# Optimization experiments

Hardware: AMD Instinct MI355X
Metric: run time of the kernel (lower is better)

## Reference

```python
import jax, jax.numpy as jnp
import numpy as np

EPS = 1e-12
SLOPE = 0.2          # LeakyReLU negative slope
N_KNN = (16, 16)     # args.n_knn
TOPK = (2, 2)        # args.topk
MHC = 32             # atten_multi_head_c

def _lin(x, w):
    # VNLinear: contract channel dim (axis 1); x: [B,Cin,3,...] w: [Cout,Cin]
    return jnp.einsum('oc,bc...->bo...', w, x)

def vn_lin_lrelu(x, w, wd):
    # VNLinearAndLeakyReLU: linear + vector-neuron leaky relu with learned direction
    x = _lin(x, w)
    d = _lin(x, wd)
    dot = (x * d).sum(2, keepdims=True)
    dsq = (d * d).sum(2, keepdims=True)
    x_neg = x - (dot / (dsq + EPS)) * d
    return SLOPE * x + (1.0 - SLOPE) * jnp.where(dot >= 0, x, x_neg)

def chnorm(x):
    # channel_equi_vec_normalize: unit 3-vectors scaled by channel-normalized norms
    n = jnp.linalg.norm(x, axis=2, keepdims=True)
    x_dir = x / jnp.maximum(n, EPS)
    cn = jnp.linalg.norm(n, axis=1, keepdims=True)
    return x_dir * (n / jnp.maximum(cn, EPS))

def get_graph_feature(x, k):
    # x: [B,C,3,N] -> [B,2C,3,N,k]; knn on flattened [B,3C,N] coordinates
    B, C, _, N = x.shape
    xf = x.reshape(B, C * 3, N)
    xx = (xf * xf).sum(1)                              # [B,N]
    inner = jnp.einsum('bdn,bdm->bnm', xf, xf)
    neg_dist = 2.0 * inner - xx[:, :, None] - xx[:, None, :]
    _, idx = jax.lax.top_k(neg_dist, k)                # [B,N,k]
    xt = jnp.transpose(x, (0, 3, 1, 2))                # [B,N,C,3]
    nbr = jax.vmap(lambda t, i: t[i])(xt, idx)         # [B,N,k,C,3]
    ctr = jnp.broadcast_to(xt[:, :, None], nbr.shape)
    feat = jnp.concatenate([nbr - ctr, ctr], axis=3)   # [B,N,k,2C,3]
    return jnp.transpose(feat, (0, 3, 4, 1, 2))

def vn_dgcnn(x, w, wd, k):
    # edge conv then mean pool over neighbors
    return vn_lin_lrelu(get_graph_feature(x, k), w, wd).mean(-1)

def cross_context(x, y, qw, qd, kw, kd, vw, vd, knn_k):
    Qx = chnorm(vn_lin_lrelu(x, qw, qd))               # [B,C,3,N]
    yg = get_graph_feature(y, knn_k)                   # [B,2C,3,N,K]
    Ky = chnorm(vn_lin_lrelu(yg, kw, kd))              # [B,C,3,N,K]
    Vy = vn_lin_lrelu(yg, vw, vd)
    qk = jnp.einsum('bcdnk,bcdn->bcnk', Ky, Qx)        # [B,C,N,K]
    B, C, N, K = qk.shape
    nh = C // MHC
    logits = qk.reshape(B, nh, MHC, N, K).sum(2) / jnp.sqrt(jnp.float32(3 * MHC))
    att = jnp.repeat(jax.nn.softmax(logits, axis=-1), MHC, axis=1)  # [B,C,N,K]
    return x + jnp.einsum('bcnk,bcdnk->bcdn', att, Vy)

def _hegn(fx, fy, blocks, h_w, h_d):
    fx = fx[:, None]   # [B,1,3,N]
    fy = fy[:, None]
    fx_blocks, fy_blocks = [], []
    for i, (dg_w, dg_d, qw, qd, kw, kd, vw, vd, gw, gd) in enumerate(blocks):
        fx = vn_dgcnn(fx, dg_w, dg_d, N_KNN[i])
        fy = vn_dgcnn(fy, dg_w, dg_d, N_KNN[i])
        fx = cross_context(fx, fy, qw, qd, kw, kd, vw, vd, N_KNN[i])
        fy = cross_context(fy, fx, qw, qd, kw, kd, vw, vd, N_KNN[i])  # uses updated fx, as in torch
        Fxg = jnp.broadcast_to(fx.mean(-1, keepdims=True), fx.shape)
        Fyg = jnp.broadcast_to(fy.mean(-1, keepdims=True), fy.shape)
        fx = vn_lin_lrelu(jnp.concatenate([fx, Fxg], 1), gw, gd)
        fy = vn_lin_lrelu(jnp.concatenate([fy, Fyg], 1), gw, gd)
        fx_par = fx.mean(1, keepdims=True)             # [B,1,3,N]
        fy_par = fy.mean(1, keepdims=True)
        fx_par = fx_par / jnp.sqrt((fx_par ** 2).sum())  # torch.norm over whole tensor
        fy_par = fy_par / jnp.sqrt((fy_par ** 2).sum())
        phi_x = jnp.einsum('bcdn,bdn->bnc', fx, fx_par[:, 0])
        phi_y = jnp.einsum('bcdn,bdn->bnc', fy, fy_par[:, 0])
        Sc = jax.nn.softmax((phi_x * phi_y).sum(-1), axis=-1)   # [B,N]
        _, idx = jax.lax.top_k(Sc, Sc.shape[1] // TOPK[i])
        fx = jnp.take_along_axis(fx, idx[:, None, None, :], axis=-1)
        fy = jnp.take_along_axis(fy, idx[:, None, None, :], axis=-1)
        fx_blocks.append(fx.mean(-1))
        fy_blocks.append(fy.mean(-1))
    Fx = vn_lin_lrelu(jnp.concatenate(fx_blocks, 1), h_w, h_d)  # [B,32,3]
    Fy = vn_lin_lrelu(jnp.concatenate(fy_blocks, 1), h_w, h_d)
    H = jnp.einsum('bcd,bce->bde', Fx, Fy)                      # [B,3,3]
    u, s, vh = jnp.linalg.svd(H, full_matrices=False)
    R = u @ jnp.swapaxes(vh, -1, -2)   # torch code computes U @ V (v = vh^T)
    S = jnp.linalg.norm(Fy, axis=1) / jnp.linalg.norm(Fx, axis=1)  # [B,3]
    return R, S

def setup_inputs():
    key = jax.random.key(0)
    ks = jax.random.split(key, 26)
    def w(k, o, i):
        return jax.random.normal(k, (o, i), dtype=jnp.float32) / np.float32(np.sqrt(i))
    B, N, C = 2, 2048, 64
    return dict(
        fx=jax.random.normal(ks[0], (B, 3, N), dtype=jnp.float32),
        fy=jax.random.normal(ks[1], (B, 3, N), dtype=jnp.float32),
        dg_w0=w(ks[2], C, 2), dg_d0=w(ks[3], C, C),
        q_w0=w(ks[4], C, C), q_d0=w(ks[5], C, C),
        k_w0=w(ks[6], C, 2 * C), k_d0=w(ks[7], C, C),
        v_w0=w(ks[8], C, 2 * C), v_d0=w(ks[9], C, C),
        g_w0=w(ks[10], C, 2 * C), g_d0=w(ks[11], C, C),
        dg_w1=w(ks[12], C, 2 * C), dg_d1=w(ks[13], C, C),
        q_w1=w(ks[14], C, C), q_d1=w(ks[15], C, C),
        k_w1=w(ks[16], C, 2 * C), k_d1=w(ks[17], C, C),
        v_w1=w(ks[18], C, 2 * C), v_d1=w(ks[19], C, C),
        g_w1=w(ks[20], C, 2 * C), g_d1=w(ks[21], C, C),
        h_w=w(ks[22], 32, 2 * C), h_d=w(ks[23], 32, 32),
    )

def reference(fx, fy, dg_w0, dg_d0, q_w0, q_d0, k_w0, k_d0, v_w0, v_d0, g_w0, g_d0,
              dg_w1, dg_d1, q_w1, q_d1, k_w1, k_d1, v_w1, v_d1, g_w1, g_d1, h_w, h_d):
    blocks = [
        (dg_w0, dg_d0, q_w0, q_d0, k_w0, k_d0, v_w0, v_d0, g_w0, g_d0),
        (dg_w1, dg_d1, q_w1, q_d1, k_w1, k_d1, v_w1, v_d1, g_w1, g_d1),
    ]
    return _hegn(fx, fy, blocks, h_w, h_d)
```

## Files before the change

kernel.cpp:

```cpp
#include <hip/hip_runtime.h>
#include <math.h>

#define SLOPE 0.2f
#define EPSV 1e-12f
#define NEGINF (-3.0e38f)

static __device__ __forceinline__ float lrelu_combine(float xv, float dvv, float dot, float dsq) {
  float xneg = xv - dot / (dsq + EPSV) * dvv;
  float w = (dot >= 0.f) ? xv : xneg;
  return SLOPE * xv + (1.f - SLOPE) * w;
}

__global__ void k_xx2(const float* __restrict__ x0, const float* __restrict__ x1,
                      float* __restrict__ xxA, float* __restrict__ xxB, int D, int N) {
  int side = blockIdx.z;
  const float* x = side ? x1 : x0;
  float* xx = side ? xxB : xxA;
  int b = blockIdx.y;
  int m = blockIdx.x * 256 + threadIdx.x;
  if (m >= N) return;
  const float* xp = x + (size_t)b * D * N + m;
  float s = 0.f;
  for (int d = 0; d < D; ++d) { float v = xp[(size_t)d * N]; s = fmaf(v, v, s); }
  xx[b * N + m] = s;
}

template <int D>
__global__ void __launch_bounds__(256) k_knn2(const float* __restrict__ x0, const float* __restrict__ x1,
                                              const float* __restrict__ xxA, const float* __restrict__ xxB,
                                              int* __restrict__ idx0, int* __restrict__ idx1, int N) {
  int side = blockIdx.z;
  const float* x = side ? x1 : x0;
  const float* xx = side ? xxB : xxA;
  int* idx = side ? idx1 : idx0;
  __shared__ float qt[D * 4];
  __shared__ float dist[4][2048];
  __shared__ float xxq[4];
  int b = blockIdx.y, tid = threadIdx.x;
  int q0 = blockIdx.x * 4;
  const float* xb = x + (size_t)b * D * N;
  for (int i = tid; i < D * 4; i += 256) qt[i] = xb[(size_t)(i >> 2) * N + q0 + (i & 3)];
  if (tid < 4) xxq[tid] = xx[b * N + q0 + tid];
  __syncthreads();
  int kouter = N >> 10;
  for (int k = 0; k < kouter; ++k) {
    int m0 = tid + (k << 10);
    float4 a0 = {0, 0, 0, 0}, a1 = {0, 0, 0, 0}, a2 = {0, 0, 0, 0}, a3 = {0, 0, 0, 0};
#pragma unroll 4
    for (int d = 0; d < D; ++d) {
      const float4 q4 = *(const float4*)&qt[d * 4];
      const float* xr = xb + (size_t)d * N + m0;
      float v0 = xr[0], v1 = xr[256], v2 = xr[512], v3 = xr[768];
      a0.x = fmaf(q4.x, v0, a0.x); a0.y = fmaf(q4.y, v0, a0.y);
      a0.z = fmaf(q4.z, v0, a0.z); a0.w = fmaf(q4.w, v0, a0.w);
      a1.x = fmaf(q4.x, v1, a1.x); a1.y = fmaf(q4.y, v1, a1.y);
      a1.z = fmaf(q4.z, v1, a1.z); a1.w = fmaf(q4.w, v1, a1.w);
      a2.x = fmaf(q4.x, v2, a2.x); a2.y = fmaf(q4.y, v2, a2.y);
      a2.z = fmaf(q4.z, v2, a2.z); a2.w = fmaf(q4.w, v2, a2.w);
      a3.x = fmaf(q4.x, v3, a3.x); a3.y = fmaf(q4.y, v3, a3.y);
      a3.z = fmaf(q4.z, v3, a3.z); a3.w = fmaf(q4.w, v3, a3.w);
    }
    const float* xxb2 = xx + b * N + m0;
    float x0v = xxb2[0], x1v = xxb2[256], x2v = xxb2[512], x3v = xxb2[768];
    dist[0][m0]       = 2.f * a0.x - xxq[0] - x0v;
    dist[1][m0]       = 2.f * a0.y - xxq[1] - x0v;
    dist[2][m0]       = 2.f * a0.z - xxq[2] - x0v;
    dist[3][m0]       = 2.f * a0.w - xxq[3] - x0v;
    dist[0][m0 + 256] = 2.f * a1.x - xxq[0] - x1v;
    dist[1][m0 + 256] = 2.f * a1.y - xxq[1] - x1v;
    dist[2][m0 + 256] = 2.f * a1.z - xxq[2] - x1v;
    dist[3][m0 + 256] = 2.f * a1.w - xxq[3] - x1v;
    dist[0][m0 + 512] = 2.f * a2.x - xxq[0] - x2v;
    dist[1][m0 + 512] = 2.f * a2.y - xxq[1] - x2v;
    dist[2][m0 + 512] = 2.f * a2.z - xxq[2] - x2v;
    dist[3][m0 + 512] = 2.f * a2.w - xxq[3] - x2v;
    dist[0][m0 + 768] = 2.f * a3.x - xxq[0] - x3v;
    dist[1][m0 + 768] = 2.f * a3.y - xxq[1] - x3v;
    dist[2][m0 + 768] = 2.f * a3.z - xxq[2] - x3v;
    dist[3][m0 + 768] = 2.f * a3.w - xxq[3] - x3v;
  }
  __syncthreads();
  int g = tid >> 6, lane = tid & 63;
  float* dr = dist[g];
  int n = q0 + g;
  int imax = N >> 8;
  int* op = idx + ((size_t)b * N + n) * 16;
  for (int r = 0; r < 16; ++r) {
    float bv = NEGINF;
    int bi = N;
    for (int i = 0; i < imax; ++i) {
      int mb = i * 256 + lane * 4;
      float4 v = *(const float4*)&dr[mb];
      if (v.x > bv) { bv = v.x; bi = mb; }
      if (v.y > bv) { bv = v.y; bi = mb + 1; }
      if (v.z > bv) { bv = v.z; bi = mb + 2; }
      if (v.w > bv) { bv = v.w; bi = mb + 3; }
    }
#pragma unroll
    for (int s = 1; s < 64; s <<= 1) {
      float ov = __shfl_xor(bv, s, 64);
      int oi = __shfl_xor(bi, s, 64);
      if (ov > bv || (ov == bv && oi < bi)) { bv = ov; bi = oi; }
    }
    if (lane == 0) { op[r] = bi; dr[bi] = NEGINF; }
  }
}

struct LinSlots {
  const float* W[5]; const float* X[5]; const float* bias[5];
  float* cm[5]; float* pm[5];
  int ws[5]; int woff[5]; int sub[5];
};

template <int KT>
__global__ void __launch_bounds__(256) k_linm(LinSlots S, int N) {
  __shared__ float wl[64 * ((KT + 3) & ~3)];
  const int KP = (KT + 3) & ~3;
  int slot = blockIdx.z >> 2;
  int oc = (blockIdx.z & 3) * 16;
  const float* W = S.W[slot];
  int ws = S.ws[slot], woff = S.woff[slot], sub = S.sub[slot];
  int tid = threadIdx.x;
  for (int i = tid; i < 64 * KT; i += 256) {
    int o = i / KT, k = i - o * KT;
    float v = W[o * ws + woff + k];
    if (sub) v -= W[o * ws + k];
    wl[o * KP + k] = v;
  }
  __syncthreads();
  int b = blockIdx.y;
  int j = blockIdx.x * 256 + tid;
  int M3 = 3 * N;
  if (j >= M3) return;
  const float* Xb = S.X[slot] + (size_t)b * KT * M3;
  float xv[KT];
#pragma unroll
  for (int k = 0; k < KT; ++k) xv[k] = Xb[(size_t)k * M3 + j];
  int d = j / N;
  const float* bias = S.bias[slot];
  float acc[16];
  if (bias) {
#pragma unroll
    for (int oo = 0; oo < 16; ++oo) acc[oo] = bias[b * 192 + (oc + oo) * 3 + d];
  } else {
#pragma unroll
    for (int oo = 0; oo < 16; ++oo) acc[oo] = 0.f;
  }
#pragma unroll
  for (int oo = 0; oo < 16; ++oo) {
    const float* wr = &wl[(oc + oo) * KP];
    float s = acc[oo];
#pragma unroll
    for (int k = 0; k < KT; ++k) s = fmaf(wr[k], xv[k], s);
    acc[oo] = s;
  }
  if (S.cm[slot]) {
    float* ob = S.cm[slot] + (size_t)b * 64 * M3;
#pragma unroll
    for (int oo = 0; oo < 16; ++oo) ob[(size_t)(oc + oo) * M3 + j] = acc[oo];
  }
  if (S.pm[slot]) {
    int n = j - d * N;
    float4* pp = (float4*)(S.pm[slot] + ((size_t)((b * N + n) * 3 + d)) * 64 + oc);
    pp[0] = make_float4(acc[0], acc[1], acc[2], acc[3]);
    pp[1] = make_float4(acc[4], acc[5], acc[6], acc[7]);
    pp[2] = make_float4(acc[8], acc[9], acc[10], acc[11]);
    pp[3] = make_float4(acc[12], acc[13], acc[14], acc[15]);
  }
}

__global__ void __launch_bounds__(256) k_edge2(const float* __restrict__ P1a, const float* __restrict__ P2a,
                                               const float* __restrict__ D1a, const float* __restrict__ D2a,
                                               const float* __restrict__ P1b, const float* __restrict__ P2b,
                                               const float* __restrict__ D1b, const float* __restrict__ D2b,
                                               const int* __restrict__ idxA, const int* __restrict__ idxB,
                                               float* __restrict__ outA, float* __restrict__ outB, int N) {
  int side = blockIdx.y;
  const float* P1 = side ? P1b : P1a;
  const float* P2 = side ? P2b : P2a;
  const float* D1 = side ? D1b : D1a;
  const float* D2 = side ? D2b : D2a;
  const int* idx = side ? idxB : idxA;
  float* out = side ? outB : outA;
  int tid = threadIdx.x;
  int p = blockIdx.x * 4 + (tid >> 6);
  int c = tid & 63;
  int b = p / N, n = p - b * N;
  size_t bn = ((size_t)(b * N + n) * 3) * 64 + c;
  float p2[3], d2[3];
#pragma unroll
  for (int d = 0; d < 3; ++d) { p2[d] = P2[bn + d * 64]; d2[d] = D2[bn + d * 64]; }
  const int* ip = idx + ((size_t)b * N + n) * 16;
  float acc0 = 0.f, acc1 = 0.f, acc2 = 0.f;
  for (int j = 0; j < 16; ++j) {
    int m = ip[j];
    size_t bm = ((size_t)(b * N + m) * 3) * 64 + c;
    float xl[3], dv[3];
#pragma unroll
    for (int d = 0; d < 3; ++d) {
      xl[d] = P1[bm + d * 64] + p2[d];
      dv[d] = D1[bm + d * 64] + d2[d];
    }
    float dot = xl[0] * dv[0] + xl[1] * dv[1] + xl[2] * dv[2];
    float dsq = dv[0] * dv[0] + dv[1] * dv[1] + dv[2] * dv[2];
    acc0 += lrelu_combine(xl[0], dv[0], dot, dsq);
    acc1 += lrelu_combine(xl[1], dv[1], dot, dsq);
    acc2 += lrelu_combine(xl[2], dv[2], dot, dsq);
  }
  size_t r0 = (size_t)((b * 64 + c) * 3) * N;
  out[r0 + n] = acc0 * (1.f / 16.f);
  out[r0 + N + n] = acc1 * (1.f / 16.f);
  out[r0 + 2 * (size_t)N + n] = acc2 * (1.f / 16.f);
}

__global__ void __launch_bounds__(256) k_qfin(const float* __restrict__ XL, const float* __restrict__ DV,
                                              float* __restrict__ outpm, int N) {
  int tid = threadIdx.x;
  int p = blockIdx.x * 4 + (tid >> 6);
  int c = tid & 63;
  int b = p / N, n = p - b * N;
  size_t bn = ((size_t)(b * N + n) * 3) * 64 + c;
  float xl[3], dv[3];
#pragma unroll
  for (int d = 0; d < 3; ++d) { xl[d] = XL[bn + d * 64]; dv[d] = DV[bn + d * 64]; }
  float dot = xl[0] * dv[0] + xl[1] * dv[1] + xl[2] * dv[2];
  float dsq = dv[0] * dv[0] + dv[1] * dv[1] + dv[2] * dv[2];
  float z[3];
#pragma unroll
  for (int d = 0; d < 3; ++d) z[d] = lrelu_combine(xl[d], dv[d], dot, dsq);
  float n2 = z[0] * z[0] + z[1] * z[1] + z[2] * z[2];
  float cn2 = n2;
#pragma unroll
  for (int s = 1; s < 64; s <<= 1) cn2 += __shfl_xor(cn2, s, 64);
  float n_o = sqrtf(n2), cn = sqrtf(cn2);
  float scl = (n_o / fmaxf(cn, EPSV)) / fmaxf(n_o, EPSV);
#pragma unroll
  for (int d = 0; d < 3; ++d) outpm[bn + d * 64] = z[d] * scl;
}

__global__ void __launch_bounds__(256) k_att(const float* __restrict__ xres,
                                             const float* __restrict__ qxpm,
                                             const float* __restrict__ KP1, const float* __restrict__ KP2,
                                             const float* __restrict__ KD1, const float* __restrict__ KD2,
                                             const float* __restrict__ VP1, const float* __restrict__ VP2,
                                             const float* __restrict__ VD1, const float* __restrict__ VD2,
                                             const int* __restrict__ idx,
                                             float* __restrict__ out, int N) {
  int tid = threadIdx.x;
  int p = blockIdx.x * 4 + (tid >> 6);
  int c = tid & 63;
  int b = p / N, n = p - b * N;
  size_t bn = ((size_t)(b * N + n) * 3) * 64 + c;
  float qv[3], kp2[3], kd2[3], vp2[3], vd2[3];
#pragma unroll
  for (int d = 0; d < 3; ++d) {
    qv[d] = qxpm[bn + d * 64];
    kp2[d] = KP2[bn + d * 64];
    kd2[d] = KD2[bn + d * 64];
    vp2[d] = VP2[bn + d * 64];
    vd2[d] = VD2[bn + d * 64];
  }
  const int* ip = idx + ((size_t)b * N + n) * 16;
  float l[16];
#pragma unroll
  for (int j = 0; j < 16; ++j) {
    int m = ip[j];
    size_t bm = ((size_t)(b * N + m) * 3) * 64 + c;
    float xl[3], dv[3];
#pragma unroll
    for (int d = 0; d < 3; ++d) {
      xl[d] = KP1[bm + d * 64] + kp2[d];
      dv[d] = KD1[bm + d * 64] + kd2[d];
    }
    float dot = xl[0] * dv[0] + xl[1] * dv[1] + xl[2] * dv[2];
    float dsq = dv[0] * dv[0] + dv[1] * dv[1] + dv[2] * dv[2];
    float z[3];
#pragma unroll
    for (int d = 0; d < 3; ++d) z[d] = lrelu_combine(xl[d], dv[d], dot, dsq);
    float n2 = z[0] * z[0] + z[1] * z[1] + z[2] * z[2];
    float cn2 = n2;
#pragma unroll
    for (int s = 1; s < 64; s <<= 1) cn2 += __shfl_xor(cn2, s, 64);
    float n_o = sqrtf(n2), cn = sqrtf(cn2);
    float scl = (n_o / fmaxf(cn, EPSV)) / fmaxf(n_o, EPSV);
    float part = (z[0] * qv[0] + z[1] * qv[1] + z[2] * qv[2]) * scl;
#pragma unroll
    for (int s = 1; s < 32; s <<= 1) part += __shfl_xor(part, s, 32);
    part = __shfl(part, 0, 32);
    l[j] = part * 0.102062072615966f;
  }
  float mx = l[0];
#pragma unroll
  for (int j = 1; j < 16; ++j) mx = fmaxf(mx, l[j]);
  float sum = 0.f;
#pragma unroll
  for (int j = 0; j < 16; ++j) { l[j] = expf(l[j] - mx); sum += l[j]; }
  float inv = 1.f / sum;
#pragma unroll
  for (int j = 0; j < 16; ++j) l[j] *= inv;
  float acc0 = 0.f, acc1 = 0.f, acc2 = 0.f;
#pragma unroll
  for (int j = 0; j < 16; ++j) {
    int m = ip[j];
    float av = l[j];
    size_t bm = ((size_t)(b * N + m) * 3) * 64 + c;
    float xl[3], dv[3];
#pragma unroll
    for (int d = 0; d < 3; ++d) {
      xl[d] = VP1[bm + d * 64] + vp2[d];
      dv[d] = VD1[bm + d * 64] + vd2[d];
    }
    float dot = xl[0] * dv[0] + xl[1] * dv[1] + xl[2] * dv[2];
    float dsq = dv[0] * dv[0] + dv[1] * dv[1] + dv[2] * dv[2];
    acc0 = fmaf(av, lrelu_combine(xl[0], dv[0], dot, dsq), acc0);
    acc1 = fmaf(av, lrelu_combine(xl[1], dv[1], dot, dsq), acc1);
    acc2 = fmaf(av, lrelu_combine(xl[2], dv[2], dot, dsq), acc2);
  }
  size_t r0 = (size_t)((b * 64 + c) * 3) * N;
  out[r0 + n] = xres[r0 + n] + acc0;
  out[r0 + N + n] = xres[r0 + N + n] + acc1;
  out[r0 + 2 * (size_t)N + n] = xres[r0 + 2 * (size_t)N + n] + acc2;
}

__global__ void __launch_bounds__(256) k_gfin(const float* __restrict__ XLa, const float* __restrict__ DVa,
                                              const float* __restrict__ XLb, const float* __restrict__ DVb,
                                              float* __restrict__ outa, float* __restrict__ outpa,
                                              float* __restrict__ outb, float* __restrict__ outpb, int N) {
  int side = blockIdx.y;
  const float* XL = side ? XLb : XLa;
  const float* DV = side ? DVb : DVa;
  float* out = side ? outb : outa;
  float* outpm = side ? outpb : outpa;
  int tid = threadIdx.x;
  int p = blockIdx.x * 4 + (tid >> 6);
  int c = tid & 63;
  int b = p / N, n = p - b * N;
  size_t bn = ((size_t)(b * N + n) * 3) * 64 + c;
  float xl[3], dv[3];
#pragma unroll
  for (int d = 0; d < 3; ++d) { xl[d] = XL[bn + d * 64]; dv[d] = DV[bn + d * 64]; }
  float dot = xl[0] * dv[0] + xl[1] * dv[1] + xl[2] * dv[2];
  float dsq = dv[0] * dv[0] + dv[1] * dv[1] + dv[2] * dv[2];
  size_t r0 = (size_t)((b * 64 + c) * 3) * N;
#pragma unroll
  for (int d = 0; d < 3; ++d) {
    float z = lrelu_combine(xl[d], dv[d], dot, dsq);
    out[r0 + (size_t)d * N + n] = z;
    outpm[bn + d * 64] = z;
  }
}

__global__ void k_gbias2(const float* __restrict__ gw, const float* __restrict__ meanX,
                         const float* __restrict__ meanY,
                         float* __restrict__ cbX, float* __restrict__ cbY) {
  int b = blockIdx.x, which = blockIdx.y, tid = threadIdx.x;
  int o = tid / 3, d = tid - o * 3;
  const float* mb = (which ? meanY : meanX) + b * 192;
  float* cb = (which ? cbY : cbX);
  float s = 0.f;
  for (int c = 0; c < 64; ++c) s = fmaf(gw[o * 128 + 64 + c], mb[c * 3 + d], s);
  cb[b * 192 + tid] = s;
}

__global__ void k_cmean2(const float* __restrict__ x1, const float* __restrict__ x2,
                         float* __restrict__ o1, float* __restrict__ o2,
                         int N, int ostride, int obase, float inv) {
  __shared__ float red[256];
  int b = blockIdx.y, cd = blockIdx.x, which = blockIdx.z, tid = threadIdx.x;
  const float* x = which ? x2 : x1;
  float* out = which ? o2 : o1;
  const float* p = x + ((size_t)b * 192 + cd) * N;
  float s = 0.f;
  for (int i = tid; i < N; i += 256) s += p[i];
  red[tid] = s;
  __syncthreads();
  for (int st = 128; st > 0; st >>= 1) {
    if (tid < st) red[tid] += red[tid + st];
    __syncthreads();
  }
  if (tid == 0) out[(size_t)b * ostride + obase + cd] = red[0] * inv;
}

__global__ void k_parmean(const float* __restrict__ fx, const float* __restrict__ fy,
                          float* __restrict__ px, float* __restrict__ py, int N, int B) {
  int gi = blockIdx.x * 256 + threadIdx.x;
  int total = B * 3 * N;
// ... 294 lines not shown
      if (idir == 1) {
        double cs = 1.0, oldcs = 1.0, sn = 0.0, oldsn = 0.0, r;
        for (int i = ll; i <= m - 1; ++i) {
          dlartg_(d[i - 1] * cs, e[i - 1], &cs, &sn, &r);
          if (i > ll) e[i - 2] = oldsn * r;
          dlartg_(oldcs * r, d[i] * sn, &oldcs, &oldsn, &d[i - 1]);
          csv[cnt] = cs; snv[cnt] = sn; ocsv[cnt] = oldcs; osnv[cnt] = oldsn; cnt++;
        }
        double hh = d[m - 1] * cs;
        d[m - 1] = hh * oldcs;
        e[m - 2] = hh * oldsn;
        for (int k = 0; k < cnt; ++k) {
          int r0 = ll - 1 + k, r1 = r0 + 1;
          for (int j = 0; j < 3; ++j) {
            double t1 = VT[r0][j], t2 = VT[r1][j];
            VT[r0][j] = snv[k] * t2 + csv[k] * t1;
            VT[r1][j] = csv[k] * t2 - snv[k] * t1;
          }
        }
        for (int k = 0; k < cnt; ++k) {
          int c0 = ll - 1 + k, c1 = c0 + 1;
          for (int i2 = 0; i2 < 3; ++i2) {
            double t1 = U[i2][c0], t2 = U[i2][c1];
            U[i2][c0] = osnv[k] * t2 + ocsv[k] * t1;
            U[i2][c1] = ocsv[k] * t2 - osnv[k] * t1;
          }
        }
        if (fabs(e[m - 2]) <= thresh) e[m - 2] = 0.0;
      } else {
        double cs = 1.0, oldcs = 1.0, sn = 0.0, oldsn = 0.0, r;
        for (int i = m; i >= ll + 1; --i) {
          dlartg_(d[i - 1] * cs, e[i - 2], &cs, &sn, &r);
          if (i < m) e[i - 1] = oldsn * r;
          dlartg_(oldcs * r, d[i - 2] * sn, &oldcs, &oldsn, &d[i - 1]);
          int k = i - ll - 1;
          csv[k] = cs; snv[k] = -sn; ocsv[k] = oldcs; osnv[k] = -oldsn; cnt++;
        }
        double hh = d[ll - 1] * cs;
        d[ll - 1] = hh * oldcs;
        e[ll - 1] = hh * oldsn;
        for (int k = cnt - 1; k >= 0; --k) {
          int r0 = ll - 1 + k, r1 = r0 + 1;
          for (int j = 0; j < 3; ++j) {
            double t1 = VT[r0][j], t2 = VT[r1][j];
            VT[r0][j] = osnv[k] * t2 + ocsv[k] * t1;
            VT[r1][j] = ocsv[k] * t2 - osnv[k] * t1;
          }
        }
        for (int k = cnt - 1; k >= 0; --k) {
          int c0 = ll - 1 + k, c1 = c0 + 1;
          for (int i2 = 0; i2 < 3; ++i2) {
            double t1 = U[i2][c0], t2 = U[i2][c1];
            U[i2][c0] = snv[k] * t2 + csv[k] * t1;
            U[i2][c1] = csv[k] * t2 - snv[k] * t1;
          }
        }
        if (fabs(e[ll - 1]) <= thresh) e[ll - 1] = 0.0;
      }
    } else {
      if (idir == 1) {
        double f = (fabs(d[ll - 1]) - shift) * (copysign(1.0, d[ll - 1]) + shift / d[ll - 1]);
        double g = e[ll - 1];
        double cosr, sinr, cosl2, sinl2, r;
        for (int i = ll; i <= m - 1; ++i) {
          dlartg_(f, g, &cosr, &sinr, &r);
          if (i > ll) e[i - 2] = r;
          f = cosr * d[i - 1] + sinr * e[i - 1];
          e[i - 1] = cosr * e[i - 1] - sinr * d[i - 1];
          g = sinr * d[i];
          d[i] = cosr * d[i];
          dlartg_(f, g, &cosl2, &sinl2, &r);
          d[i - 1] = r;
          f = cosl2 * e[i - 1] + sinl2 * d[i];
          d[i] = cosl2 * d[i] - sinl2 * e[i - 1];
          if (i < m - 1) {
            g = sinl2 * e[i];
            e[i] = cosl2 * e[i];
          }
          csv[cnt] = cosr; snv[cnt] = sinr; ocsv[cnt] = cosl2; osnv[cnt] = sinl2; cnt++;
        }
        e[m - 2] = f;
        for (int k = 0; k < cnt; ++k) {
          int r0 = ll - 1 + k, r1 = r0 + 1;
          for (int j = 0; j < 3; ++j) {
            double t1 = VT[r0][j], t2 = VT[r1][j];
            VT[r0][j] = snv[k] * t2 + csv[k] * t1;
            VT[r1][j] = csv[k] * t2 - snv[k] * t1;
          }
        }
        for (int k = 0; k < cnt; ++k) {
          int c0 = ll - 1 + k, c1 = c0 + 1;
          for (int i2 = 0; i2 < 3; ++i2) {
            double t1 = U[i2][c0], t2 = U[i2][c1];
            U[i2][c0] = osnv[k] * t2 + ocsv[k] * t1;
            U[i2][c1] = ocsv[k] * t2 - osnv[k] * t1;
          }
        }
        if (fabs(e[m - 2]) <= thresh) e[m - 2] = 0.0;
      } else {
        double f = (fabs(d[m - 1]) - shift) * (copysign(1.0, d[m - 1]) + shift / d[m - 1]);
        double g = e[m - 2];
        for (int i = m; i >= ll + 1; --i) {
          double cosr, sinr, cosl2, sinl2, r;
          dlartg_(f, g, &cosr, &sinr, &r);
          if (i < m) e[i - 1] = r;
          f = cosr * d[i - 1] + sinr * e[i - 2];
          e[i - 2] = cosr * e[i - 2] - sinr * d[i - 1];
          g = sinr * d[i - 2];
          d[i - 2] = cosr * d[i - 2];
          dlartg_(f, g, &cosl2, &sinl2, &r);
          d[i - 1] = r;
          f = cosl2 * e[i - 2] + sinl2 * d[i - 2];
          d[i - 2] = cosl2 * d[i - 2] - sinl2 * e[i - 2];
          if (i > ll + 1) {
            g = sinl2 * e[i - 3];
            e[i - 3] = cosl2 * e[i - 3];
          }
          int k = i - ll - 1;
          ocsv[k] = cosl2; osnv[k] = -sinl2; csv[k] = cosr; snv[k] = -sinr; cnt++;
        }
        e[ll - 1] = f;
        for (int k = cnt - 1; k >= 0; --k) {
          int r0 = ll - 1 + k, r1 = r0 + 1;
          for (int j = 0; j < 3; ++j) {
            double t1 = VT[r0][j], t2 = VT[r1][j];
            VT[r0][j] = snv[k] * t2 + csv[k] * t1;
            VT[r1][j] = csv[k] * t2 - snv[k] * t1;
          }
        }
        for (int k = cnt - 1; k >= 0; --k) {
          int c0 = ll - 1 + k, c1 = c0 + 1;
          for (int i2 = 0; i2 < 3; ++i2) {
            double t1 = U[i2][c0], t2 = U[i2][c1];
            U[i2][c0] = osnv[k] * t2 + ocsv[k] * t1;
            U[i2][c1] = ocsv[k] * t2 - osnv[k] * t1;
          }
        }
        if (fabs(e[ll - 1]) <= thresh) e[ll - 1] = 0.0;
      }
    }
  }
  for (int i = 0; i < n; ++i)
    if (d[i] < 0.0) { d[i] = -d[i]; for (int j = 0; j < 3; ++j) VT[i][j] = -VT[i][j]; }
  for (int i = 1; i <= n - 1; ++i) {
    int isub = 1; double smn = d[0];
    for (int j = 2; j <= n + 1 - i; ++j)
      if (d[j - 1] <= smn) { isub = j; smn = d[j - 1]; }
    if (isub != n + 1 - i) {
      int a = isub - 1, b2 = n - i;
      double t = d[a]; d[a] = d[b2]; d[b2] = t;
      for (int j = 0; j < 3; ++j) { t = VT[a][j]; VT[a][j] = VT[b2][j]; VT[b2][j] = t; }
      for (int j = 0; j < 3; ++j) { t = U[j][a]; U[j][a] = U[j][b2]; U[j][b2] = t; }
    }
  }
}

__global__ void k_svd(const float* __restrict__ Fx, const float* __restrict__ Fy,
                      float* __restrict__ out, int B) {
  int b = blockIdx.x;
  if (threadIdx.x != 0) return;
  double A[3][3];
  for (int d = 0; d < 3; ++d)
    for (int e = 0; e < 3; ++e) {
      double s = 0.0;
      for (int c = 0; c < 32; ++c)
        s += (double)Fx[((size_t)b * 32 + c) * 3 + d] * (double)Fy[((size_t)b * 32 + c) * 3 + e];
      A[d][e] = s;
    }
  double dg[3], eg[2], tauq0, tauq1, taup0;
  double v1_1 = 0, v1_2 = 0, v2_1 = 0, w1 = 0;
  {
    double alpha = A[0][0];
    double xn = sqrt(A[1][0] * A[1][0] + A[2][0] * A[2][0]);
    if (xn == 0.0) { tauq0 = 0.0; dg[0] = alpha; }
    else {
      double beta = -copysign(sqrt(alpha * alpha + xn * xn), alpha);
      tauq0 = (beta - alpha) / beta;
      double scal = 1.0 / (alpha - beta);
      v1_1 = A[1][0] * scal; v1_2 = A[2][0] * scal;
      dg[0] = beta;
    }
    for (int j = 1; j < 3; ++j) {
      double w = A[0][j] + v1_1 * A[1][j] + v1_2 * A[2][j];
      w *= tauq0;
      A[0][j] -= w; A[1][j] -= w * v1_1; A[2][j] -= w * v1_2;
    }
  }
  {
    double alpha = A[0][1];
    double xn = fabs(A[0][2]);
    if (xn == 0.0) { taup0 = 0.0; eg[0] = alpha; }
    else {
      double beta = -copysign(sqrt(alpha * alpha + xn * xn), alpha);
      taup0 = (beta - alpha) / beta;
      w1 = A[0][2] / (alpha - beta);
      eg[0] = beta;
    }
    for (int i = 1; i < 3; ++i) {
      double t = A[i][1] + w1 * A[i][2];
      t *= taup0;
      A[i][1] -= t; A[i][2] -= t * w1;
    }
  }
  {
    double alpha = A[1][1];
    double xn = fabs(A[2][1]);
    if (xn == 0.0) { tauq1 = 0.0; dg[1] = alpha; }
    else {
      double beta = -copysign(sqrt(alpha * alpha + xn * xn), alpha);
      tauq1 = (beta - alpha) / beta;
      v2_1 = A[2][1] / (alpha - beta);
      dg[1] = beta;
    }
    double w = A[1][2] + v2_1 * A[2][2];
    w *= tauq1;
    A[1][2] -= w; A[2][2] -= w * v2_1;
  }
  eg[1] = A[1][2];
  dg[2] = A[2][2];
  double U[3][3] = {{1, 0, 0}, {0, 1, 0}, {0, 0, 1}};
  double VT[3][3] = {{1, 0, 0}, {0, 1, 0}, {0, 0, 1}};
  dbdsqr3(dg, eg, VT, U);
  for (int j = 0; j < 3; ++j) {
    double w = U[1][j] + v2_1 * U[2][j];
    w *= tauq1;
    U[1][j] -= w; U[2][j] -= w * v2_1;
  }
  for (int j = 0; j < 3; ++j) {
    double w = U[0][j] + v1_1 * U[1][j] + v1_2 * U[2][j];
    w *= tauq0;
    U[0][j] -= w; U[1][j] -= w * v1_1; U[2][j] -= w * v1_2;
  }
  for (int r = 0; r < 3; ++r) {
    double t = VT[r][1] + w1 * VT[r][2];
    t *= taup0;
    VT[r][1] -= t; VT[r][2] -= t * w1;
  }
  for (int i = 0; i < 3; ++i)
    for (int j = 0; j < 3; ++j) {
      double r = 0;
      for (int k = 0; k < 3; ++k) r += U[i][k] * VT[j][k];
      out[b * 9 + i * 3 + j] = (float)r;
    }
  for (int dd = 0; dd < 3; ++dd) {
    float sx = 0.f, sy = 0.f;
    for (int c = 0; c < 32; ++c) {
      float vx = Fx[((size_t)b * 32 + c) * 3 + dd];
      float vy = Fy[((size_t)b * 32 + c) * 3 + dd];
      sx = fmaf(vx, vx, sx);
      sy = fmaf(vy, vy, sy);
    }
    out[B * 9 + b * 3 + dd] = sqrtf(sy) / sqrtf(sx);
  }
}

extern "C" void kernel_launch(void* const* d_in, const int* in_sizes, int n_in,
                              void* d_out, int out_size, void* d_ws, size_t ws_size,
                              hipStream_t stream) {
  (void)in_sizes; (void)n_in; (void)out_size; (void)ws_size;
  const int B = 2, N0 = 2048;
  const float* W[24];
  for (int i = 0; i < 24; ++i) W[i] = (const float*)d_in[i];

  float* ws = (float*)d_ws;
  const size_t P = (size_t)B * 64 * 3 * 2048;
  float* bufA = ws;
  float* bufB = bufA + P;
  float* bufC = bufB + P;
  float* bufD = bufC + P;
  float* bufApm = bufD + P;
  float* bufBpm = bufApm + P;
  float* qxpm = bufBpm + P;
  float* C1 = qxpm + P;
  float* C2 = C1 + P;
  float* C3 = C2 + P;
  float* C4 = C3 + P;
  float* C5 = C4 + P;
  float* M1 = C5 + P;
  float* M2 = M1 + P;
  float* M3 = M2 + P;
  float* M4 = M3 + P;
  float* M5 = M4 + P;
  float* M6 = M5 + P;
  float* M7 = M6 + P;
  float* M8 = M7 + P;
  float* M9 = M8 + P;
  float* M10 = M9 + P;
  float* px = M10 + P;
  float* py = px + 12288;
  float* dps = py + 12288;
  float* xx0 = dps + 4096;
  float* xx1 = xx0 + 4096;
  float* meanX = xx1 + 4096;
  float* meanY = meanX + 384;
  float* cbX = meanY + 384;
  float* cbY = cbX + 384;
  float* blkX = cbY + 384;
  float* blkY = blkX + 768;
  float* Fxb = blkY + 768;
  float* Fyb = Fxb + 192;
  int* idxA = (int*)(Fyb + 192);
  int* idxB = idxA + 65536;
  int* sel = idxB + 65536;

  auto knn2s = [&](const float* xa, const float* xb2, int D, int N, int* ia, int* ib, int ns) {
    k_xx2<<<dim3((N + 255) / 256, B, ns), 256, 0, stream>>>(xa, xb2, xx0, xx1, D, N);
    dim3 g2(N / 4, B, ns);
    if (D == 192) k_knn2<192><<<g2, 256, 0, stream>>>(xa, xb2, xx0, xx1, ia, ib, N);
    else          k_knn2<3><<<g2, 256, 0, stream>>>(xa, xb2, xx0, xx1, ia, ib, N);
  };

  const float* fx = W[0];
  const float* fy = W[1];
  int N = N0;
  for (int blk = 0; blk < 2; ++blk) {
    int D = (blk == 0) ? 3 : 192;
    const float* dgw = W[blk ? 12 : 2]; const float* dgd = W[blk ? 13 : 3];
    const float* qw  = W[blk ? 14 : 4]; const float* qd  = W[blk ? 15 : 5];
    const float* kw  = W[blk ? 16 : 6]; const float* kd  = W[blk ? 17 : 7];
    const float* vw  = W[blk ? 18 : 8]; const float* vd  = W[blk ? 19 : 9];
    const float* gw  = W[blk ? 20 : 10]; const float* gd = W[blk ? 21 : 11];
    dim3 gP(B * N / 4);
    dim3 gL((3 * N + 255) / 256, B, 1);

    knn2s(fx, fy, D, N, idxA, idxB, 2);
    {
      LinSlots s{};
      int wsd = (blk == 0) ? 2 : 128;
      int off2 = (blk == 0) ? 1 : 64;
      const float* Xs[4] = {fx, fx, fy, fy};
      float* cms[4] = {C1, C2, C3, C4};
      float* pms[4] = {M1, M2, M3, M4};
      for (int i = 0; i < 4; ++i) {
        s.W[i] = dgw; s.X[i] = Xs[i]; s.bias[i] = nullptr;
        s.cm[i] = cms[i]; s.pm[i] = pms[i];
        s.ws[i] = wsd; s.woff[i] = (i & 1) ? off2 : 0; s.sub[i] = (i & 1);
      }
      gL.z = 16;
      if (blk == 0) k_linm<1><<<gL, 256, 0, stream>>>(s, N);
      else          k_linm<64><<<gL, 256, 0, stream>>>(s, N);
    }
    {
      LinSlots s{};
      const float* Xs[4] = {C1, C2, C3, C4};
      float* pms[4] = {M5, M6, M7, M8};
      for (int i = 0; i < 4; ++i) {
        s.W[i] = dgd; s.X[i] = Xs[i]; s.bias[i] = nullptr;
        s.cm[i] = nullptr; s.pm[i] = pms[i];
        s.ws[i] = 64; s.woff[i] = 0; s.sub[i] = 0;
      }
      gL.z = 16;
      k_linm<64><<<gL, 256, 0, stream>>>(s, N);
    }
    k_edge2<<<dim3(B * N / 4, 2), 256, 0, stream>>>(M1, M2, M5, M6, M3, M4, M7, M8,
                                                    idxA, idxB, bufA, bufB, N);

    knn2s(bufB, bufB, 192, N, idxB, idxB, 1);
    {
      LinSlots s{};
      const float* Wm[5] = {qw, kw, kw, vw, vw};
      const float* Xs[5] = {bufA, bufB, bufB, bufB, bufB};
      float* cms[5] = {C1, C2, C3, C4, C5};
      float* pms[5] = {M1, M3, M4, M5, M6};
      int wss[5] = {64, 128, 128, 128, 128};
      int offs[5] = {0, 0, 64, 0, 64};
      int subs[5] = {0, 0, 1, 0, 1};
      for (int i = 0; i < 5; ++i) {
        s.W[i] = Wm[i]; s.X[i] = Xs[i]; s.bias[i] = nullptr;
        s.cm[i] = cms[i]; s.pm[i] = pms[i];
        s.ws[i] = wss[i]; s.woff[i] = offs[i]; s.sub[i] = subs[i];
      }
      gL.z = 20;
      k_linm<64><<<gL, 256, 0, stream>>>(s, N);
    }
    {
      LinSlots s{};
      const float* Wm[5] = {qd, kd, kd, vd, vd};
      const float* Xs[5] = {C1, C2, C3, C4, C5};
      float* pms[5] = {M2, M7, M8, M9, M10};
      for (int i = 0; i < 5; ++i) {
        s.W[i] = Wm[i]; s.X[i] = Xs[i]; s.bias[i] = nullptr;
        s.cm[i] = nullptr; s.pm[i] = pms[i];
        s.ws[i] = 64; s.woff[i] = 0; s.sub[i] = 0;
      }
      gL.z = 20;
      k_linm<64><<<gL, 256, 0, stream>>>(s, N);
    }
    k_qfin<<<gP, 256, 0, stream>>>(M1, M2, qxpm, N);
    k_att<<<gP, 256, 0, stream>>>(bufA, qxpm, M3, M4, M7, M8, M5, M6, M9, M10, idxB, bufC, N);

    knn2s(bufC, bufC, 192, N, idxA, idxA, 1);
    {
      LinSlots s{};
      const float* Wm[5] = {qw, kw, kw, vw, vw};
      const float* Xs[5] = {bufB, bufC, bufC, bufC, bufC};
      float* cms[5] = {C1, C2, C3, C4, C5};
      float* pms[5] = {M1, M3, M4, M5, M6};
      int wss[5] = {64, 128, 128, 128, 128};
      int offs[5] = {0, 0, 64, 0, 64};
      int subs[5] = {0, 0, 1, 0, 1};
      for (int i = 0; i < 5; ++i) {
        s.W[i] = Wm[i]; s.X[i] = Xs[i]; s.bias[i] = nullptr;
        s.cm[i] = cms[i]; s.pm[i] = pms[i];
        s.ws[i] = wss[i]; s.woff[i] = offs[i]; s.sub[i] = subs[i];
      }
      gL.z = 20;
      k_linm<64><<<gL, 256, 0, stream>>>(s, N);
    }
    {
      LinSlots s{};
      const float* Wm[5] = {qd, kd, kd, vd, vd};
      const float* Xs[5] = {C1, C2, C3, C4, C5};
      float* pms[5] = {M2, M7, M8, M9, M10};
      for (int i = 0; i < 5; ++i) {
        s.W[i] = Wm[i]; s.X[i] = Xs[i]; s.bias[i] = nullptr;
        s.cm[i] = nullptr; s.pm[i] = pms[i];
        s.ws[i] = 64; s.woff[i] = 0; s.sub[i] = 0;
      }
      gL.z = 20;
      k_linm<64><<<gL, 256, 0, stream>>>(s, N);
    }
    k_qfin<<<gP, 256, 0, stream>>>(M1, M2, qxpm, N);
    k_att<<<gP, 256, 0, stream>>>(bufB, qxpm, M3, M4, M7, M8, M5, M6, M9, M10, idxA, bufD, N);

    k_cmean2<<<dim3(192, B, 2), 256, 0, stream>>>(bufC, bufD, meanX, meanY, N, 192, 0, 1.f / (float)N);
    k_gbias2<<<dim3(B, 2), 192, 0, stream>>>(gw, meanX, meanY, cbX, cbY);
    {
      LinSlots s{};
      const float* Xs[2] = {bufC, bufD};
      const float* bs[2] = {cbX, cbY};
      float* cms[2] = {C1, C2};
      float* pms[2] = {M1, M2};
      for (int i = 0; i < 2; ++i) {
        s.W[i] = gw; s.X[i] = Xs[i]; s.bias[i] = bs[i];
        s.cm[i] = cms[i]; s.pm[i] = pms[i];
        s.ws[i] = 128; s.woff[i] = 0; s.sub[i] = 0;
      }
      gL.z = 8;
      k_linm<64><<<gL, 256, 0, stream>>>(s, N);
    }
    {
      LinSlots s{};
      const float* Xs[2] = {C1, C2};
      float* pms[2] = {M3, M4};
      for (int i = 0; i < 2; ++i) {
        s.W[i] = gd; s.X[i] = Xs[i]; s.bias[i] = nullptr;
        s.cm[i] = nullptr; s.pm[i] = pms[i];
        s.ws[i] = 64; s.woff[i] = 0; s.sub[i] = 0;
      }
      gL.z = 8;
      k_linm<64><<<gL, 256, 0, stream>>>(s, N);
    }
    k_gfin<<<dim3(B * N / 4, 2), 256, 0, stream>>>(M1, M3, M2, M4, bufA, bufApm, bufB, bufBpm, N);

    int Nh = N / 2;
    k_parmean<<<dim3((B * 3 * N + 255) / 256), 256, 0, stream>>>(bufA, bufB, px, py, N, B);
    k_dotphi<<<dim3((B * N + 255) / 256), 256, 0, stream>>>(bufA, bufB, px, py, dps, N, B);
    k_topsel<<<dim3(B), 1024, 0, stream>>>(dps, sel, N, Nh);
    k_gather<<<dim3(B * Nh / 4), 256, 0, stream>>>(bufApm, bufBpm, sel, bufC, bufD, N, Nh);
    k_cmean2<<<dim3(192, B, 2), 256, 0, stream>>>(bufC, bufD, blkX, blkY, Nh, 384, blk * 192, 1.f / (float)Nh);
    fx = bufC; fy = bufD;
    N = Nh;
  }
  k_head<<<dim3(2, B), 96, 0, stream>>>(blkX, blkY, W[22], W[23], Fxb, Fyb);
  k_svd<<<dim3(B), 64, 0, stream>>>(Fxb, Fyb, (float*)d_out, B);
}
```

Measured before the change: 1.380 ms.

## Split 192-dim kNN into tiled Gram-matrix kernel plus separate top-k selection

After: 1.419 ms. 2.8% more time.

```diff
diff --git a/kernel.cpp b/kernel.cpp
--- a/kernel.cpp
+++ b/kernel.cpp
@@ -46,7 +46,7 @@
   for (int k = 0; k < kouter; ++k) {
     int m0 = tid + (k << 10);
     float4 a0 = {0, 0, 0, 0}, a1 = {0, 0, 0, 0}, a2 = {0, 0, 0, 0}, a3 = {0, 0, 0, 0};
-#pragma unroll 4
+#pragma unroll
     for (int d = 0; d < D; ++d) {
       const float4 q4 = *(const float4*)&qt[d * 4];
       const float* xr = xb + (size_t)d * N + m0;
@@ -82,6 +82,108 @@
   __syncthreads();
   int g = tid >> 6, lane = tid & 63;
   float* dr = dist[g];
+  int n = q0 + g;
+  int imax = N >> 8;
+  int* op = idx + ((size_t)b * N + n) * 16;
+  for (int r = 0; r < 16; ++r) {
+    float bv = NEGINF;
+    int bi = N;
+    for (int i = 0; i < imax; ++i) {
+      int mb = i * 256 + lane * 4;
+      float4 v = *(const float4*)&dr[mb];
+      if (v.x > bv) { bv = v.x; bi = mb; }
+      if (v.y > bv) { bv = v.y; bi = mb + 1; }
+      if (v.z > bv) { bv = v.z; bi = mb + 2; }
+      if (v.w > bv) { bv = v.w; bi = mb + 3; }
+    }
+#pragma unroll
+    for (int s = 1; s < 64; s <<= 1) {
+      float ov = __shfl_xor(bv, s, 64);
+      int oi = __shfl_xor(bi, s, 64);
+      if (ov > bv || (ov == bv && oi < bi)) { bv = ov; bi = oi; }
+    }
+    if (lane == 0) { op[r] = bi; dr[bi] = NEGINF; }
+  }
+}
+
+template <int D>
+__global__ void __launch_bounds__(256) k_gram(const float* __restrict__ x0, const float* __restrict__ x1,
+                                              const float* __restrict__ xxA, const float* __restrict__ xxB,
+                                              float* __restrict__ dist, int N) {
+  int side = blockIdx.z;
+  const float* x = side ? x1 : x0;
+  const float* xx = side ? xxB : xxA;
+  __shared__ float sq[16][64];
+  __shared__ float sm[16][64];
+  int qtiles = N >> 6;
+  int b = blockIdx.y / qtiles;
+  int qt = blockIdx.y - b * qtiles;
+  int m0 = blockIdx.x << 6;
+  int q0 = qt << 6;
+  int tid = threadIdx.x;
+  int tmg = tid & 15, tqg = tid >> 4;
+  const float* xb = x + (size_t)b * D * N;
+  float acc[16];
+#pragma unroll
+  for (int i = 0; i < 16; ++i) acc[i] = 0.f;
+  for (int dc = 0; dc < D; dc += 16) {
+    for (int i = tid; i < 1024; i += 256) {
+      int dd = i >> 6, c = i & 63;
+      sq[dd][c] = xb[(size_t)(dc + dd) * N + q0 + c];
+      sm[dd][c] = xb[(size_t)(dc + dd) * N + m0 + c];
+    }
+    __syncthreads();
+#pragma unroll
+    for (int dd = 0; dd < 16; ++dd) {
+      float4 qv = *(const float4*)&sq[dd][tqg * 4];
+      float4 mv = *(const float4*)&sm[dd][tmg * 4];
+      acc[0]  = fmaf(qv.x, mv.x, acc[0]);
+      acc[1]  = fmaf(qv.x, mv.y, acc[1]);
+      acc[2]  = fmaf(qv.x, mv.z, acc[2]);
+      acc[3]  = fmaf(qv.x, mv.w, acc[3]);
+      acc[4]  = fmaf(qv.y, mv.x, acc[4]);
+      acc[5]  = fmaf(qv.y, mv.y, acc[5]);
+      acc[6]  = fmaf(qv.y, mv.z, acc[6]);
+      acc[7]  = fmaf(qv.y, mv.w, acc[7]);
+      acc[8]  = fmaf(qv.z, mv.x, acc[8]);
+      acc[9]  = fmaf(qv.z, mv.y, acc[9]);
+      acc[10] = fmaf(qv.z, mv.z, acc[10]);
+      acc[11] = fmaf(qv.z, mv.w, acc[11]);
+      acc[12] = fmaf(qv.w, mv.x, acc[12]);
+      acc[13] = fmaf(qv.w, mv.y, acc[13]);
+      acc[14] = fmaf(qv.w, mv.z, acc[14]);
+      acc[15] = fmaf(qv.w, mv.w, acc[15]);
+    }
+    __syncthreads();
+  }
+  float4 xxm = *(const float4*)&xx[b * N + m0 + tmg * 4];
+#pragma unroll
+  for (int qi = 0; qi < 4; ++qi) {
+    int q = q0 + tqg * 4 + qi;
+    float xq = xx[b * N + q];
+    float4 o;
+    o.x = 2.f * acc[qi * 4 + 0] - xq - xxm.x;
+    o.y = 2.f * acc[qi * 4 + 1] - xq - xxm.y;
+    o.z = 2.f * acc[qi * 4 + 2] - xq - xxm.z;
+    o.w = 2.f * acc[qi * 4 + 3] - xq - xxm.w;
+    *(float4*)&dist[((size_t)((side * 2 + b) * N + q)) * N + m0 + tmg * 4] = o;
+  }
+}
+
+__global__ void __launch_bounds__(256) k_sel(const float* __restrict__ dist,
+                                             int* __restrict__ idx0, int* __restrict__ idx1, int N) {
+  int side = blockIdx.z;
+  int* idx = side ? idx1 : idx0;
+  __shared__ float dr4[4][2048];
+  int b = blockIdx.y, tid = threadIdx.x;
+  int q0 = blockIdx.x * 4;
+  for (int g2 = 0; g2 < 4; ++g2) {
+    const float* row = dist + ((size_t)((side * 2 + b) * N + q0 + g2)) * N;
+    for (int m = tid; m < N; m += 256) dr4[g2][m] = row[m];
+  }
+  __syncthreads();
+  int g = tid >> 6, lane = tid & 63;
+  float* dr = dr4[g];
   int n = q0 + g;
   int imax = N >> 8;
   int* op = idx + ((size_t)b * N + n) * 16;
@@ -982,19 +1084,24 @@
   int* idxA = (int*)(Fyb + 192);
   int* idxB = idxA + 65536;
   int* sel = idxB + 65536;
-
-  auto knn2s = [&](const float* xa, const float* xb2, int D, int N, int* ia, int* ib, int ns) {
-    k_xx2<<<dim3((N + 255) / 256, B, ns), 256, 0, stream>>>(xa, xb2, xx0, xx1, D, N);
+  float* distb = C1;
+
+  auto knn3 = [&](const float* xa, const float* xb2, int N, int* ia, int* ib, int ns) {
+    k_xx2<<<dim3((N + 255) / 256, B, ns), 256, 0, stream>>>(xa, xb2, xx0, xx1, 3, N);
     dim3 g2(N / 4, B, ns);
-    if (D == 192) k_knn2<192><<<g2, 256, 0, stream>>>(xa, xb2, xx0, xx1, ia, ib, N);
-    else          k_knn2<3><<<g2, 256, 0, stream>>>(xa, xb2, xx0, xx1, ia, ib, N);
+    k_knn2<3><<<g2, 256, 0, stream>>>(xa, xb2, xx0, xx1, ia, ib, N);
+  };
+  auto knn192 = [&](const float* xa, const float* xb2, int N, int* ia, int* ib, int ns) {
+    k_xx2<<<dim3((N + 255) / 256, B, ns), 256, 0, stream>>>(xa, xb2, xx0, xx1, 192, N);
+    int qtiles = N >> 6;
+    k_gram<192><<<dim3(qtiles, B * qtiles, ns), 256, 0, stream>>>(xa, xb2, xx0, xx1, distb, N);
+    k_sel<<<dim3(N / 4, B, ns), 256, 0, stream>>>(distb, ia, ib, N);
   };
 
   const float* fx = W[0];
   const float* fy = W[1];
   int N = N0;
   for (int blk = 0; blk < 2; ++blk) {
-    int D = (blk == 0) ? 3 : 192;
     const float* dgw = W[blk ? 12 : 2]; const float* dgd = W[blk ? 13 : 3];
     const float* qw  = W[blk ? 14 : 4]; const float* qd  = W[blk ? 15 : 5];
     const float* kw  = W[blk ? 16 : 6]; const float* kd  = W[blk ? 17 : 7];
@@ -1003,7 +1110,8 @@
     dim3 gP(B * N / 4);
     dim3 gL((3 * N + 255) / 256, B, 1);
 
-    knn2s(fx, fy, D, N, idxA, idxB, 2);
+    if (blk == 0) knn3(fx, fy, N, idxA, idxB, 2);
+    else          knn192(fx, fy, N, idxA, idxB, 2);
     {
       LinSlots s{};
       int wsd = (blk == 0) ? 2 : 128;
@@ -1035,7 +1143,7 @@
     k_edge2<<<dim3(B * N / 4, 2), 256, 0, stream>>>(M1, M2, M5, M6, M3, M4, M7, M8,
                                                     idxA, idxB, bufA, bufB, N);
 
-    knn2s(bufB, bufB, 192, N, idxB, idxB, 1);
+    knn192(bufB, bufB, N, idxB, idxB, 1);
     {
       LinSlots s{};
       const float* Wm[5] = {qw, kw, kw, vw, vw};
@@ -1069,7 +1177,7 @@
     k_qfin<<<gP, 256, 0, stream>>>(M1, M2, qxpm, N);
     k_att<<<gP, 256, 0, stream>>>(bufA, qxpm, M3, M4, M7, M8, M5, M6, M9, M10, idxB, bufC, N);
 
-    knn2s(bufC, bufC, 192, N, idxA, idxA, 1);
+    knn192(bufC, bufC, N, idxA, idxA, 1);
     {
       LinSlots s{};
       const float* Wm[5] = {qw, kw, kw, vw, vw};
```
